# Performance work log

Hardware: AMD Instinct MI355X
Metric: run time of the kernel (lower is better)

Reference implementation:

```python
import jax, jax.numpy as jnp
import numpy as np

NC = 80          # class_num
THRESH = 0.5     # objectness threshold (forward arg `thresh`)
IOU_T = 0.3      # NMS IoU threshold (utils.nms(boxes_c, 0.3))
K = 512          # fixed candidate budget per image (jit-safe replacement for nonzero)


def _decode(out, t, anchors):
    """_filter + _parse for one scale. out: (B, 3*(5+NC), H, W) -> boxes (B, H*W*3, 6), conf (B, H*W*3).
    Box columns: x1, y1, x2, y2, conf, cls."""
    B, C, H, W = out.shape
    o = out.transpose(0, 2, 3, 1).reshape(B, H, W, 3, 5 + NC)
    txy = jax.nn.sigmoid(o[..., 0:2])          # sigmoid on tx, ty
    conf = jax.nn.sigmoid(o[..., 4])           # sigmoid on objectness
    gy = jnp.arange(H, dtype=out.dtype)[:, None, None]   # grid row index (idxs[:,1])
    gx = jnp.arange(W, dtype=out.dtype)[None, :, None]   # grid col index (idxs[:,2])
    cy = (gy + txy[..., 1]) * t
    cx = (gx + txy[..., 0]) * t
    w = anchors[:, 0] * jnp.exp(o[..., 2])     # anchors broadcast over anchor axis
    h = anchors[:, 1] * jnp.exp(o[..., 3])
    cls = jnp.argmax(o[..., 5:], axis=-1).astype(out.dtype)
    boxes = jnp.stack([cx - w / 2, cy - h / 2, cx + w / 2, cy + h / 2, conf, cls], axis=-1)
    return boxes.reshape(B, -1, 6), conf.reshape(B, -1)


def _iou(b):
    """Pairwise IoU. b: (B, K, 4) -> (B, K, K)."""
    x1, y1, x2, y2 = b[..., 0], b[..., 1], b[..., 2], b[..., 3]
    area = (x2 - x1) * (y2 - y1)
    ix1 = jnp.maximum(x1[:, :, None], x1[:, None, :])
    iy1 = jnp.maximum(y1[:, :, None], y1[:, None, :])
    ix2 = jnp.minimum(x2[:, :, None], x2[:, None, :])
    iy2 = jnp.minimum(y2[:, :, None], y2[:, None, :])
    inter = jnp.maximum(ix2 - ix1, 0.0) * jnp.maximum(iy2 - iy1, 0.0)
    return inter / (area[:, :, None] + area[:, None, :] - inter + 1e-9)


def setup_inputs() -> dict:
    key = jax.random.key(0)
    k1, k2, k3 = jax.random.split(key, 3)
    B, C = 32, 3 * (5 + NC)
    return {
        "out13": jax.random.normal(k1, (B, C, 13, 13), jnp.float32),
        "out26": jax.random.normal(k2, (B, C, 26, 26), jnp.float32),
        "out52": jax.random.normal(k3, (B, C, 52, 52), jnp.float32),
        "anchors13": jnp.array([[116.0, 90.0], [156.0, 198.0], [373.0, 326.0]], jnp.float32),
        "anchors26": jnp.array([[30.0, 61.0], [62.0, 45.0], [59.0, 119.0]], jnp.float32),
        "anchors52": jnp.array([[10.0, 13.0], [16.0, 30.0], [33.0, 23.0]], jnp.float32),
    }


def reference(out13, out26, out52, anchors13, anchors26, anchors52):
    b13, c13 = _decode(out13, 32.0, anchors13)
    b26, c26 = _decode(out26, 16.0, anchors26)
    b52, c52 = _decode(out52, 8.0, anchors52)
    boxes = jnp.concatenate([b13, b26, b52], axis=1)   # (B, N, 6), N = 3549*3
    conf = jnp.concatenate([c13, c26, c52], axis=1)    # (B, N)
    B = boxes.shape[0]

    # threshold filter (conf > thresh) realized as masked top-K (jit-safe nonzero)
    scores = jnp.where(conf > THRESH, conf, -1.0)
    vals, idx = jax.lax.top_k(scores, K)               # sorted descending, as utils.nms expects
    bk = jnp.take_along_axis(boxes, idx[..., None], axis=1)   # (B, K, 6)
    valid = vals > THRESH                              # (B, K)

    # per-class greedy NMS
    iou = _iou(bk[..., :4])                            # (B, K, K)
    same_cls = bk[..., 5][:, :, None] == bk[..., 5][:, None, :]
    suppress = same_cls & (iou > IOU_T)

    def step(keep, i):
        sup_i = jnp.any(keep & suppress[:, i, :], axis=-1)
        keep = keep.at[:, i].set(valid[:, i] & ~sup_i)
        return keep, None

    keep, _ = jax.lax.scan(step, jnp.zeros((B, K), dtype=bool), jnp.arange(K))
    # (B, K, 7): x1, y1, x2, y2, conf, cls, keep_flag
    return jnp.concatenate([bk, keep[..., None].astype(bk.dtype)], axis=-1)
```

## Files before the change

kernel.cpp:

```cpp
#include <hip/hip_runtime.h>
#include <stdint.h>

#define NC13 507
#define NC26 2028
#define NC52 8112
#define NCAND 10647
#define KSEL 512
#define POOLCAP 4096
#define SUPW 17
#define CMW 17

__device__ __forceinline__ unsigned long long cand_key(
    int i, int b,
    const float* __restrict__ in13,
    const float* __restrict__ in26,
    const float* __restrict__ in52)
{
    const float* in; int HW, base;
    if (i < NC13)              { in = in13; HW = 169;  base = 0; }
    else if (i < NC13 + NC26)  { in = in26; HW = 676;  base = NC13; }
    else                       { in = in52; HW = 2704; base = NC13 + NC26; }
    const int within = i - base;
    const int a  = within / HW;
    const int hw = within - a * HW;
    const float xo = in[((size_t)b * 255 + (size_t)a * 85 + 4) * HW + hw];
    const int n = base + hw * 3 + a;
    const unsigned long long low = (unsigned long long)(0x3FFFu - (unsigned)n);
    return (xo > 0.0f)
        ? ((1ull << 63) | ((unsigned long long)__float_as_uint(xo) << 32) | low)
        : low;
}

__global__ __launch_bounds__(1024) void selscore_kernel(
    const float* __restrict__ in13,
    const float* __restrict__ in26,
    const float* __restrict__ in52,
    int* __restrict__ selidx,
    int* __restrict__ selv)
{
    __shared__ unsigned int hist[4096];
    __shared__ unsigned long long pool[POOLCAP];
    __shared__ unsigned int cnt;
    __shared__ unsigned long long sh_prefix;
    __shared__ unsigned long long sh_tmin;
    __shared__ int sh_krem;
    __shared__ int sh_shift;
    __shared__ int sh_break;

    const int b = blockIdx.x;
    const int tid = threadIdx.x;

    if (tid == 0) { sh_prefix = 0; sh_krem = KSEL; sh_shift = 52; sh_break = 0; cnt = 0; }
    __syncthreads();

    while (true) {
        const int shift = sh_shift;
        const unsigned long long prefix = sh_prefix;
        const int krem = sh_krem;
        __syncthreads();
        for (int i = tid; i < 4096; i += 1024) hist[i] = 0;
        __syncthreads();
        for (int i = tid; i < NCAND; i += 1024) {
            const unsigned long long k = cand_key(i, b, in13, in26, in52);
            const bool ok = (shift == 52) || ((k >> (shift + 12)) == prefix);
            if (ok) atomicAdd(&hist[(unsigned)((k >> shift) & 0xFFFull)], 1u);
        }
        __syncthreads();
        if (tid < 64) {
            unsigned int s = 0;
            for (int q = 0; q < 64; ++q) s += hist[tid * 64 + q];
            unsigned int suf = s;
            for (int off = 1; off < 64; off <<= 1) {
                const unsigned int v = __shfl_down(suf, off);
                if (tid + off < 64) suf += v;
            }
            const unsigned long long ball = __ballot(suf >= (unsigned)krem);
            const int lstar = 63 - __clzll(ball);
            const unsigned int base = (lstar < 63) ? __shfl(suf, lstar + 1) : 0u;
            const unsigned int wv = hist[lstar * 64 + (63 - tid)];
            unsigned int pv = wv;
            for (int off = 1; off < 64; off <<= 1) {
                const unsigned int v = __shfl_up(pv, off);
                if (tid >= (unsigned)off) pv += v;
            }
            const unsigned long long b2 = __ballot(base + pv >= (unsigned)krem);
            const int mstar = __ffsll(b2) - 1;
            const unsigned int pvm = __shfl(pv, mstar);
            const unsigned int wvm = __shfl(wv, mstar);
            if (tid == 0) {
                const int dstar = lstar * 64 + (63 - mstar);
                const unsigned long long np = (prefix << 12) | (unsigned long long)dstar;
                const int Albl = (int)(base + pvm - wvm);
                const int Cpool = (KSEL - krem) + Albl + (int)wvm;
                sh_prefix = np;
                sh_krem = krem - Albl;
                if (Cpool <= POOLCAP || shift == 4) {
                    sh_break = 1;
                    sh_tmin = np << shift;
                } else {
                    sh_shift = shift - 12;
                }
            }
        }
        __syncthreads();
        if (sh_break) break;
    }
    const unsigned long long tmin = sh_tmin;

    for (int i = tid; i < NCAND; i += 1024) {
        const unsigned long long k = cand_key(i, b, in13, in26, in52);
        if (k >= tmin) {
            const unsigned int p = atomicAdd(&cnt, 1u);
            if (p < POOLCAP) pool[p] = k;
        }
    }
    __syncthreads();
    const int C = ((int)cnt < POOLCAP) ? (int)cnt : POOLCAP;

    for (int p = tid; p < C; p += 1024) {
        const unsigned long long k = pool[p];
        int r = 0;
        for (int j = 0; j < C; ++j) r += (pool[j] > k) ? 1 : 0;
        if (r < KSEL) {
            const int idx = 0x3FFF - (int)(k & 0x3FFFull);
            selidx[(size_t)b * KSEL + r] = idx;
            selv[(size_t)b * KSEL + r]   = (int)(k >> 63);
        }
    }
}

__global__ __launch_bounds__(256) void decode_all_kernel(
    const float* __restrict__ in13,
    const float* __restrict__ in26,
    const float* __restrict__ in52,
    const float* __restrict__ a13,
    const float* __restrict__ a26,
    const float* __restrict__ a52,
    float* __restrict__ boxesAll)
{
    const int chunk = blockIdx.x;
    const int a = blockIdx.y;
    const int b = blockIdx.z;
    const float* in; const float* anch; int H, base, hw0; float ts;
    if (chunk == 0)      { in = in13; anch = a13; H = 13; ts = 32.f; base = 0;           hw0 = 0; }
    else if (chunk <= 3) { in = in26; anch = a26; H = 26; ts = 16.f; base = NC13;        hw0 = (chunk - 1) * 256; }
    else                 { in = in52; anch = a52; H = 52; ts = 8.f;  base = NC13 + NC26; hw0 = (chunk - 4) * 256; }
    const int HW = H * H;
    const int hw = hw0 + threadIdx.x;
    if (hw >= HW) return;
    const int h = hw / H, w = hw - h * H;
    const float* p = in + ((size_t)b * 255 + (size_t)a * 85) * HW + hw;

    const float tx = p[0];
    const float ty = p[(size_t)HW];
    const float tw = p[(size_t)2 * HW];
    const float th = p[(size_t)3 * HW];
    const float xo = p[(size_t)4 * HW];

    unsigned long long k = 0;
    #pragma unroll
    for (int c = 0; c < 80; ++c) {
        const float v = p[(size_t)(5 + c) * HW];
        unsigned int u = __float_as_uint(v);
        u = (u & 0x80000000u) ? ~u : (u | 0x80000000u);
        const unsigned long long kk =
            ((unsigned long long)u << 32) | (unsigned long long)(127 - c);
        if (kk > k) k = kk;
    }
    const int cls = 127 - (int)(k & 0xFFull);

    const float sx   = 1.0f / (1.0f + expf(-tx));
    const float sy   = 1.0f / (1.0f + expf(-ty));
    const float conf = 1.0f / (1.0f + expf(-xo));
    const float cx = ((float)w + sx) * ts;
    const float cy = ((float)h + sy) * ts;
    const float bw = anch[2 * a + 0] * expf(tw);
    const float bh = anch[2 * a + 1] * expf(th);

    const int i = base + a * HW + hw;
    float* o = boxesAll + ((size_t)b * NCAND + i) * 6;
    o[0] = cx - bw * 0.5f; o[1] = cy - bh * 0.5f;
    o[2] = cx + bw * 0.5f; o[3] = cy + bh * 0.5f;
    o[4] = conf; o[5] = (float)cls;
}

__global__ __launch_bounds__(512) void nms_kernel(
    const float* __restrict__ boxesAll,
    const int* __restrict__ selidx,
    const int* __restrict__ selv,
    float* __restrict__ out)
{
    __shared__ float X1[KSEL], Y1[KSEL], X2[KSEL], Y2[KSEL], AR[KSEL];
    __shared__ int CLS[KSEL];
    __shared__ unsigned int CM[80 * CMW];
    __shared__ unsigned int SUP[KSEL * SUPW];
    __shared__ unsigned int KEEP[16];
    __shared__ int shV;

    const int b = blockIdx.x;
    const int tid = threadIdx.x;

    const int n = selidx[(size_t)b * KSEL + tid];
    int base, HW;
    if (n < NC13)             { base = 0;           HW = 169; }
    else if (n < NC13 + NC26) { base = NC13;        HW = 676; }
    else                      { base = NC13 + NC26; HW = 2704; }
    const int within = n - base;
    const int hw = within / 3, a = within - 3 * hw;
    const int i = base + a * HW + hw;
    const float* src = boxesAll + ((size_t)b * NCAND + i) * 6;
    const float x1 = src[0], y1 = src[1], x2 = src[2], y2 = src[3];
    const float conf = src[4], clsf = src[5];
    const float ar = (x2 - x1) * (y2 - y1);
    const int ci = (int)clsf;
    X1[tid] = x1; Y1[tid] = y1; X2[tid] = x2; Y2[tid] = y2;
    AR[tid] = ar; CLS[tid] = ci;
    const int v = selv[(size_t)b * KSEL + tid];
    if (tid == 0) shV = 0;
    for (int q = tid; q < 80 * CMW; q += KSEL) CM[q] = 0;
    __syncthreads();

    atomicOr(&CM[ci * CMW + (tid >> 5)], 1u << (tid & 31));
    const unsigned long long bal = __ballot(v != 0);
    if ((tid & 63) == 0) atomicAdd(&shV, __popcll(bal));
    __syncthreads();

    for (int wj = 0; wj < 16; ++wj) {
        unsigned int m = CM[ci * CMW + wj];
        unsigned int bits = 0;
        while (m) {
            const int bit = __ffs(m) - 1;
            m &= m - 1;
            const int j = wj * 32 + bit;
            const float iw = fminf(x2, X2[j]) - fmaxf(x1, X1[j]);
            const float ih = fminf(y2, Y2[j]) - fmaxf(y1, Y1[j]);
            if (iw > 0.0f && ih > 0.0f) {
                const float inter = iw * ih;
                if (inter > 0.3f * (ar + AR[j] - inter + 1e-9f))
                    bits |= (1u << bit);
            }
        }
        SUP[tid * SUPW + wj] = bits;
    }
    __syncthreads();

    if (tid < 64) {
        const int V = shV;
        unsigned int keepw = 0;
        unsigned int buf[16];
        #pragma unroll
        for (int r = 0; r < 16; ++r)
            buf[r] = (tid < 16) ? SUP[r * SUPW + tid] : 0u;
        for (int g = 0; g < 32; ++g) {
            unsigned int nbuf[16] = {0};
            if (g < 31) {
                #pragma unroll
                for (int r = 0; r < 16; ++r)
                    nbuf[r] = (tid < 16) ? SUP[((g + 1) * 16 + r) * SUPW + tid] : 0u;
            }
            #pragma unroll
            for (int r = 0; r < 16; ++r) {
                const int ii = g * 16 + r;
                const bool anysup = __any((keepw & buf[r]) != 0u);
                const bool ki = (ii < V) && !anysup;
                if (ki && tid == (ii >> 5)) keepw |= (1u << (ii & 31));
            }
            #pragma unroll
            for (int r = 0; r < 16; ++r) buf[r] = nbuf[r];
        }
        if (tid < 16) KEEP[tid] = keepw;
    }
    __syncthreads();

    const float kf = ((KEEP[tid >> 5] >> (tid & 31)) & 1u) ? 1.0f : 0.0f;
    float* dst = out + ((size_t)b * KSEL + tid) * 7;
    dst[0] = x1; dst[1] = y1; dst[2] = x2;
    dst[3] = y2; dst[4] = conf; dst[5] = clsf;
    dst[6] = kf;
}

extern "C" void kernel_launch(void* const* d_in, const int* in_sizes, int n_in,
                              void* d_out, int out_size, void* d_ws, size_t ws_size,
                              hipStream_t stream)
{
    (void)n_in; (void)out_size; (void)ws_size;
    const float* in13 = (const float*)d_in[0];
    const float* in26 = (const float*)d_in[1];
    const float* in52 = (const float*)d_in[2];
    const float* a13  = (const float*)d_in[3];
    const float* a26  = (const float*)d_in[4];
    const float* a52  = (const float*)d_in[5];
    float* out = (float*)d_out;
    const int B = in_sizes[0] / (255 * 169);

    char* w = (char*)d_ws;
    int* selidx = (int*)w;  w += ((size_t)B * KSEL * sizeof(int) + 255) & ~(size_t)255;
    int* selv   = (int*)w;  w += ((size_t)B * KSEL * sizeof(int) + 255) & ~(size_t)255;
    float* boxesAll = (float*)w;
    w += ((size_t)B * NCAND * 6 * sizeof(float) + 255) & ~(size_t)255;

    selscore_kernel<<<dim3(B), 1024, 0, stream>>>(in13, in26, in52, selidx, selv);
    decode_all_kernel<<<dim3(15, 3, B), 256, 0, stream>>>(
        in13, in26, in52, a13, a26, a52, boxesAll);
    nms_kernel<<<dim3(B), 512, 0, stream>>>(boxesAll, selidx, selv, out);
}
```

Baseline: 80.30 us.

## Merge selection and decode into one launch with float2 decode and valid-only histogram

Combines the top-K selection kernel and the box decode kernel into one grid. The first B blocks run selection and the remaining blocks decode, so the two stages overlap on the GPU and one launch is saved. Decode now uses float2 loads so each thread handles two cells, and argmax uses a plain float compare instead of packed 64-bit keys. Selection first counts valid candidates and, when at least K exist, leaves invalid ones out of the histograms, which can reduce radix passes. The trade-off is 1024-thread decode blocks, and every block reserves the selection kernel's large shared-memory footprint, which may lower occupancy.

```diff
diff --git a/kernel.cpp b/kernel.cpp
--- a/kernel.cpp
+++ b/kernel.cpp
@@ -9,6 +9,7 @@
 #define POOLCAP 4096
 #define SUPW 17
 #define CMW 17
+#define DECB 6
 
 __device__ __forceinline__ unsigned long long cand_key(
     int i, int b,
@@ -31,157 +32,202 @@
         : low;
 }
 
-__global__ __launch_bounds__(1024) void selscore_kernel(
-    const float* __restrict__ in13,
-    const float* __restrict__ in26,
-    const float* __restrict__ in52,
-    int* __restrict__ selidx,
-    int* __restrict__ selv)
-{
-    __shared__ unsigned int hist[4096];
-    __shared__ unsigned long long pool[POOLCAP];
-    __shared__ unsigned int cnt;
-    __shared__ unsigned long long sh_prefix;
-    __shared__ unsigned long long sh_tmin;
-    __shared__ int sh_krem;
-    __shared__ int sh_shift;
-    __shared__ int sh_break;
-
-    const int b = blockIdx.x;
-    const int tid = threadIdx.x;
-
-    if (tid == 0) { sh_prefix = 0; sh_krem = KSEL; sh_shift = 52; sh_break = 0; cnt = 0; }
-    __syncthreads();
-
-    while (true) {
-        const int shift = sh_shift;
-        const unsigned long long prefix = sh_prefix;
-        const int krem = sh_krem;
-        __syncthreads();
-        for (int i = tid; i < 4096; i += 1024) hist[i] = 0;
-        __syncthreads();
-        for (int i = tid; i < NCAND; i += 1024) {
-            const unsigned long long k = cand_key(i, b, in13, in26, in52);
-            const bool ok = (shift == 52) || ((k >> (shift + 12)) == prefix);
-            if (ok) atomicAdd(&hist[(unsigned)((k >> shift) & 0xFFFull)], 1u);
-        }
-        __syncthreads();
-        if (tid < 64) {
-            unsigned int s = 0;
-            for (int q = 0; q < 64; ++q) s += hist[tid * 64 + q];
-            unsigned int suf = s;
-            for (int off = 1; off < 64; off <<= 1) {
-                const unsigned int v = __shfl_down(suf, off);
-                if (tid + off < 64) suf += v;
-            }
-            const unsigned long long ball = __ballot(suf >= (unsigned)krem);
-            const int lstar = 63 - __clzll(ball);
-            const unsigned int base = (lstar < 63) ? __shfl(suf, lstar + 1) : 0u;
-            const unsigned int wv = hist[lstar * 64 + (63 - tid)];
-            unsigned int pv = wv;
-            for (int off = 1; off < 64; off <<= 1) {
-                const unsigned int v = __shfl_up(pv, off);
-                if (tid >= (unsigned)off) pv += v;
-            }
-            const unsigned long long b2 = __ballot(base + pv >= (unsigned)krem);
-            const int mstar = __ffsll(b2) - 1;
-            const unsigned int pvm = __shfl(pv, mstar);
-            const unsigned int wvm = __shfl(wv, mstar);
-            if (tid == 0) {
-                const int dstar = lstar * 64 + (63 - mstar);
-                const unsigned long long np = (prefix << 12) | (unsigned long long)dstar;
-                const int Albl = (int)(base + pvm - wvm);
-                const int Cpool = (KSEL - krem) + Albl + (int)wvm;
-                sh_prefix = np;
-                sh_krem = krem - Albl;
-                if (Cpool <= POOLCAP || shift == 4) {
-                    sh_break = 1;
-                    sh_tmin = np << shift;
-                } else {
-                    sh_shift = shift - 12;
-                }
-            }
-        }
-        __syncthreads();
-        if (sh_break) break;
-    }
-    const unsigned long long tmin = sh_tmin;
-
-    for (int i = tid; i < NCAND; i += 1024) {
-        const unsigned long long k = cand_key(i, b, in13, in26, in52);
-        if (k >= tmin) {
-            const unsigned int p = atomicAdd(&cnt, 1u);
-            if (p < POOLCAP) pool[p] = k;
-        }
-    }
-    __syncthreads();
-    const int C = ((int)cnt < POOLCAP) ? (int)cnt : POOLCAP;
-
-    for (int p = tid; p < C; p += 1024) {
-        const unsigned long long k = pool[p];
-        int r = 0;
-        for (int j = 0; j < C; ++j) r += (pool[j] > k) ? 1 : 0;
-        if (r < KSEL) {
-            const int idx = 0x3FFF - (int)(k & 0x3FFFull);
-            selidx[(size_t)b * KSEL + r] = idx;
-            selv[(size_t)b * KSEL + r]   = (int)(k >> 63);
-        }
-    }
-}
-
-__global__ __launch_bounds__(256) void decode_all_kernel(
+struct SelShared {
+    unsigned int hist[4096];
+    unsigned long long pool[POOLCAP];
+    unsigned int cnt;
+    unsigned long long prefix;
+    unsigned long long tmin;
+    int krem, shift, brk, V;
+};
+
+__device__ __forceinline__ void decode_write(
+    float* __restrict__ o, int w, int h, float ts,
+    float tx, float ty, float tw, float th, float xo,
+    float aw, float ah, int cls)
+{
+    const float sx   = 1.0f / (1.0f + expf(-tx));
+    const float sy   = 1.0f / (1.0f + expf(-ty));
+    const float conf = 1.0f / (1.0f + expf(-xo));
+    const float cx = ((float)w + sx) * ts;
+    const float cy = ((float)h + sy) * ts;
+    const float bw = aw * expf(tw);
+    const float bh = ah * expf(th);
+    o[0] = cx - bw * 0.5f; o[1] = cy - bh * 0.5f;
+    o[2] = cx + bw * 0.5f; o[3] = cy + bh * 0.5f;
+    o[4] = conf; o[5] = (float)cls;
+}
+
+__global__ __launch_bounds__(1024) void main_kernel(
     const float* __restrict__ in13,
     const float* __restrict__ in26,
     const float* __restrict__ in52,
     const float* __restrict__ a13,
     const float* __restrict__ a26,
     const float* __restrict__ a52,
+    int B,
+    int* __restrict__ selidx,
+    int* __restrict__ selv,
     float* __restrict__ boxesAll)
 {
-    const int chunk = blockIdx.x;
-    const int a = blockIdx.y;
-    const int b = blockIdx.z;
-    const float* in; const float* anch; int H, base, hw0; float ts;
-    if (chunk == 0)      { in = in13; anch = a13; H = 13; ts = 32.f; base = 0;           hw0 = 0; }
-    else if (chunk <= 3) { in = in26; anch = a26; H = 26; ts = 16.f; base = NC13;        hw0 = (chunk - 1) * 256; }
-    else                 { in = in52; anch = a52; H = 52; ts = 8.f;  base = NC13 + NC26; hw0 = (chunk - 4) * 256; }
-    const int HW = H * H;
-    const int hw = hw0 + threadIdx.x;
-    if (hw >= HW) return;
-    const int h = hw / H, w = hw - h * H;
-    const float* p = in + ((size_t)b * 255 + (size_t)a * 85) * HW + hw;
-
-    const float tx = p[0];
-    const float ty = p[(size_t)HW];
-    const float tw = p[(size_t)2 * HW];
-    const float th = p[(size_t)3 * HW];
-    const float xo = p[(size_t)4 * HW];
-
-    unsigned long long k = 0;
-    #pragma unroll
-    for (int c = 0; c < 80; ++c) {
-        const float v = p[(size_t)(5 + c) * HW];
-        unsigned int u = __float_as_uint(v);
-        u = (u & 0x80000000u) ? ~u : (u | 0x80000000u);
-        const unsigned long long kk =
-            ((unsigned long long)u << 32) | (unsigned long long)(127 - c);
-        if (kk > k) k = kk;
-    }
-    const int cls = 127 - (int)(k & 0xFFull);
-
-    const float sx   = 1.0f / (1.0f + expf(-tx));
-    const float sy   = 1.0f / (1.0f + expf(-ty));
-    const float conf = 1.0f / (1.0f + expf(-xo));
-    const float cx = ((float)w + sx) * ts;
-    const float cy = ((float)h + sy) * ts;
-    const float bw = anch[2 * a + 0] * expf(tw);
-    const float bh = anch[2 * a + 1] * expf(th);
-
-    const int i = base + a * HW + hw;
-    float* o = boxesAll + ((size_t)b * NCAND + i) * 6;
-    o[0] = cx - bw * 0.5f; o[1] = cy - bh * 0.5f;
-    o[2] = cx + bw * 0.5f; o[3] = cy + bh * 0.5f;
-    o[4] = conf; o[5] = (float)cls;
+    __shared__ __align__(16) char smem_raw[sizeof(SelShared)];
+    const int bid = blockIdx.x;
+    const int tid = threadIdx.x;
+
+    if (bid < B) {
+        SelShared& S = *reinterpret_cast<SelShared*>(smem_raw);
+        const int b = bid;
+        if (tid == 0) { S.cnt = 0; S.prefix = 0; S.krem = KSEL; S.shift = 52; S.brk = 0; S.V = 0; }
+        __syncthreads();
+
+        for (int i = tid; i < NCAND; i += 1024) {
+            const unsigned long long k = cand_key(i, b, in13, in26, in52);
+            const unsigned long long bal = __ballot((k >> 63) != 0ull);
+            if ((tid & 63) == 0) atomicAdd(&S.V, (int)__popcll(bal));
+        }
+        __syncthreads();
+        const bool include = (S.V < KSEL);
+
+        while (true) {
+            const int shift = S.shift;
+            const unsigned long long prefix = S.prefix;
+            const int krem = S.krem;
+            __syncthreads();
+            for (int i = tid; i < 4096; i += 1024) S.hist[i] = 0;
+            __syncthreads();
+            for (int i = tid; i < NCAND; i += 1024) {
+                const unsigned long long k = cand_key(i, b, in13, in26, in52);
+                const bool part = include || ((k >> 63) != 0ull);
+                const bool ok = part &&
+                    ((shift == 52) || ((k >> (shift + 12)) == prefix));
+                if (ok) atomicAdd(&S.hist[(unsigned)((k >> shift) & 0xFFFull)], 1u);
+            }
+            __syncthreads();
+            if (tid < 64) {
+                unsigned int s = 0;
+                for (int q = 0; q < 64; ++q) s += S.hist[tid * 64 + q];
+                unsigned int suf = s;
+                for (int off = 1; off < 64; off <<= 1) {
+                    const unsigned int v = __shfl_down(suf, off);
+                    if (tid + off < 64) suf += v;
+                }
+                const unsigned long long ball = __ballot(suf >= (unsigned)krem);
+                const int lstar = 63 - __clzll(ball);
+                const unsigned int base = (lstar < 63) ? __shfl(suf, lstar + 1) : 0u;
+                const unsigned int wv = S.hist[lstar * 64 + (63 - tid)];
+                unsigned int pv = wv;
+                for (int off = 1; off < 64; off <<= 1) {
+                    const unsigned int v = __shfl_up(pv, off);
+                    if (tid >= (unsigned)off) pv += v;
+                }
+                const unsigned long long b2 = __ballot(base + pv >= (unsigned)krem);
+                const int mstar = __ffsll(b2) - 1;
+                const unsigned int pvm = __shfl(pv, mstar);
+                const unsigned int wvm = __shfl(wv, mstar);
+                if (tid == 0) {
+                    const int dstar = lstar * 64 + (63 - mstar);
+                    const unsigned long long np = (prefix << 12) | (unsigned long long)dstar;
+                    const int Albl = (int)(base + pvm - wvm);
+                    const int Cpool = (KSEL - krem) + Albl + (int)wvm;
+                    S.prefix = np;
+                    S.krem = krem - Albl;
+                    if (Cpool <= POOLCAP || shift == 4) {
+                        S.brk = 1;
+                        S.tmin = np << shift;
+                    } else {
+                        S.shift = shift - 12;
+                    }
+                }
+            }
+            __syncthreads();
+            if (S.brk) break;
+        }
+        const unsigned long long tmin = S.tmin;
+
+        for (int i = tid; i < NCAND; i += 1024) {
+            const unsigned long long k = cand_key(i, b, in13, in26, in52);
+            if (k >= tmin) {
+                const unsigned int p = atomicAdd(&S.cnt, 1u);
+                if (p < POOLCAP) S.pool[p] = k;
+            }
+        }
+        __syncthreads();
+        const int C = ((int)S.cnt < POOLCAP) ? (int)S.cnt : POOLCAP;
+
+        for (int p = tid; p < C; p += 1024) {
+            const unsigned long long k = S.pool[p];
+            int r = 0;
+            for (int j = 0; j < C; ++j) r += (S.pool[j] > k) ? 1 : 0;
+            if (r < KSEL) {
+                const int idx = 0x3FFF - (int)(k & 0x3FFFull);
+                selidx[(size_t)b * KSEL + r] = idx;
+                selv[(size_t)b * KSEL + r]   = (int)(k >> 63);
+            }
+        }
+        return;
+    }
+
+    const int d = bid - B;
+    const int b = d / DECB;
+    const int role = d - b * DECB;
+
+    if (role == 0) {
+        if (tid >= NC13) return;
+        const int HW = 169;
+        const int a = tid / HW, hw = tid - a * HW;
+        const int h = hw / 13, w = hw - h * 13;
+        const float* p = in13 + ((size_t)b * 255 + (size_t)a * 85) * HW + hw;
+        float best = p[(size_t)5 * HW]; int bi = 0;
+        #pragma unroll 16
+        for (int c = 1; c < 80; ++c) {
+            const float v = p[(size_t)(5 + c) * HW];
+            if (v > best) { best = v; bi = c; }
+        }
+        const int i = a * HW + hw;
+        decode_write(boxesAll + ((size_t)b * NCAND + i) * 6, w, h, 32.f,
+                     p[0], p[(size_t)HW], p[(size_t)2 * HW], p[(size_t)3 * HW],
+                     p[(size_t)4 * HW], a13[2 * a], a13[2 * a + 1], bi);
+        return;
+    }
+
+    const float* in; const float* anch; int HW, base, idx2; float ts; int Hdim;
+    if (role == 1) {
+        if (tid >= NC26 / 2) return;
+        in = in26; anch = a26; HW = 676;  base = NC13; ts = 16.f; Hdim = 26; idx2 = tid;
+    } else {
+        idx2 = (role - 2) * 1024 + tid;
+        if (idx2 >= NC52 / 2) return;
+        in = in52; anch = a52; HW = 2704; base = NC13 + NC26; ts = 8.f; Hdim = 52;
+    }
+    const int HW2 = HW / 2;
+    const int a = idx2 / HW2;
+    const int hw = (idx2 - a * HW2) * 2;
+    const float2* p2 = reinterpret_cast<const float2*>(
+        in + ((size_t)b * 255 + (size_t)a * 85) * HW + hw);
+
+    const float2 txv = p2[0];
+    const float2 tyv = p2[(size_t)HW2];
+    const float2 twv = p2[(size_t)2 * HW2];
+    const float2 thv = p2[(size_t)3 * HW2];
+    const float2 xov = p2[(size_t)4 * HW2];
+
+    float2 best = p2[(size_t)5 * HW2];
+    int bix = 0, biy = 0;
+    #pragma unroll 16
+    for (int c = 1; c < 80; ++c) {
+        const float2 v = p2[(size_t)(5 + c) * HW2];
+        if (v.x > best.x) { best.x = v.x; bix = c; }
+        if (v.y > best.y) { best.y = v.y; biy = c; }
+    }
+
+    const int h0 = hw / Hdim, w0 = hw - h0 * Hdim;
+    const int hw1 = hw + 1;
+    const int h1 = hw1 / Hdim, w1 = hw1 - h1 * Hdim;
+    const float aw = anch[2 * a], ah = anch[2 * a + 1];
+    const int i0 = base + a * HW + hw;
+    float* o = boxesAll + ((size_t)b * NCAND + i0) * 6;
+    decode_write(o,     w0, h0, ts, txv.x, tyv.x, twv.x, thv.x, xov.x, aw, ah, bix);
+    decode_write(o + 6, w1, h1, ts, txv.y, tyv.y, twv.y, thv.y, xov.y, aw, ah, biy);
 }
 
 __global__ __launch_bounds__(512) void nms_kernel(
@@ -299,8 +345,7 @@
     float* boxesAll = (float*)w;
     w += ((size_t)B * NCAND * 6 * sizeof(float) + 255) & ~(size_t)255;
 
-    selscore_kernel<<<dim3(B), 1024, 0, stream>>>(in13, in26, in52, selidx, selv);
-    decode_all_kernel<<<dim3(15, 3, B), 256, 0, stream>>>(
-        in13, in26, in52, a13, a26, a52, boxesAll);
+    main_kernel<<<dim3(B * (1 + DECB)), 1024, 0, stream>>>(
+        in13, in26, in52, a13, a26, a52, B, selidx, selv, boxesAll);
     nms_kernel<<<dim3(B), 512, 0, stream>>>(boxesAll, selidx, selv, out);
 }
```

After: 69.23 us. 13.8% less time.
